# Performance work log

Measured on AMD Instinct MI355X. Metric: run time of the kernel, lower is better.

Reference implementation:

```python
import jax, jax.numpy as jnp
import numpy as np

NPOINT, RADIUS, SIGMA, K = 1024, 0.1, 0.05, 32
KDE_K = 128  # N_points default of kernel_density_estimation_ball


def setup_inputs() -> dict:
    key = jax.random.key(0)
    ks = jax.random.split(key, 9)
    B, N, C = 4, 4096, 16

    def glorot(k, shape):
        fan_in, fan_out = shape
        return jax.random.normal(k, shape, jnp.float32) * jnp.sqrt(2.0 / (fan_in + fan_out))

    return {
        'xyz': jax.random.uniform(ks[0], (B, N, 3), jnp.float32),      # unit cube
        'feature': jax.random.normal(ks[1], (B, N, C), jnp.float32),
        'w_mlp0': glorot(ks[2], (3 + C, 128)),
        'w_mlp1': glorot(ks[3], (128, 128)),
        'w_mlp2': glorot(ks[4], (128, 256)),
        'w_wn': glorot(ks[5], (3, 32)),
        'w_nl0': glorot(ks[6], (1, 16)),
        'w_nl1': glorot(ks[7], (16, 1)),
        'w_np': glorot(ks[8], (32, 256)),
    }


def _pdist2(a, b):
    # squared pairwise distances [B, M, N]
    return (jnp.sum(a * a, -1)[:, :, None] + jnp.sum(b * b, -1)[:, None, :]
            - 2.0 * jnp.einsum('bmd,bnd->bmn', a, b))


def _fps(xyz, npoint):
    # farthest point sampling, seeded at index 0 (matches CUDA op semantics)
    B, N, _ = xyz.shape

    def step(carry, _):
        min_d, last = carry
        p = jnp.take_along_axis(xyz, last[:, None, None], axis=1)  # [B,1,3]
        d = jnp.sum((xyz - p) ** 2, -1)                            # [B,N]
        min_d = jnp.minimum(min_d, d)
        nxt = jnp.argmax(min_d, axis=1).astype(jnp.int32)
        return (min_d, nxt), nxt

    init = (jnp.full((B, N), jnp.inf, xyz.dtype), jnp.zeros((B,), jnp.int32))
    _, rest = jax.lax.scan(step, init, None, length=npoint - 1)
    return jnp.concatenate([jnp.zeros((B, 1), jnp.int32), rest.T], axis=1)  # [B,npoint]


def _ball_query(xyz, radius, k):
    # first-k-in-index-order neighbors with d2 < r^2, padded with first hit
    B, N, _ = xyz.shape
    d2 = _pdist2(xyz, xyz)
    in_ball = d2 < radius * radius                 # self always included
    j = jnp.arange(N, dtype=jnp.int32)
    keys = jnp.where(in_ball, j, j + N)            # in-ball indices sort first
    _, idx = jax.lax.top_k(-keys, k)               # k smallest keys -> positions j
    cnt = jnp.minimum(jnp.sum(in_ball, axis=-1), k)            # [B,N]
    valid = jnp.arange(k) < cnt[..., None]
    idx = jnp.where(valid, idx, idx[..., :1])
    return idx, cnt


def _kde_ball(xyz, radius, sigma, kde_k):
    idx, cnt = _ball_query(xyz, radius, kde_k)     # [B,N,kde_k], [B,N]
    b_ix = jnp.arange(xyz.shape[0])[:, None, None]
    g = xyz[b_ix, idx] - xyz[:, :, None, :]        # [B,N,kde_k,3]
    R = jnp.sqrt(jnp.float32(sigma))
    quad = jnp.sum(jnp.square(g / R), axis=-1)     # [B,N,kde_k]
    mvn = jnp.exp(-0.5 * quad - 3.0 * jnp.log(R) - 1.5 * jnp.log(2.0 * 3.1415926))
    first = mvn[..., :1]
    total = jnp.sum(mvn, axis=-1, keepdims=True)
    cntf = cnt.astype(xyz.dtype)[..., None]
    total = total - first * (jnp.float32(kde_k) - cntf)  # remove padded duplicates
    return total / cntf                             # [B,N,1]


def _knn(k, src, q):
    d2 = _pdist2(q, src)                            # [B,P,N]
    _, idx = jax.lax.top_k(-d2, k)                  # ascending distance
    return idx


def _forward(xyz, feature, w_mlp0, w_mlp1, w_mlp2, w_wn, w_nl0, w_nl1, w_np):
    B = xyz.shape[0]
    conv = lambda x, w: jax.nn.relu(jnp.einsum('bpkc,cf->bpkf', x, w))  # bias-free 1x1 conv

    fps_idx = _fps(xyz, NPOINT)
    new_xyz = jnp.take_along_axis(xyz, fps_idx[..., None], axis=1)      # [B,P,3]

    knn_idx = _knn(K, xyz, new_xyz)                                      # [B,P,K]
    b_ix = jnp.arange(B)[:, None, None]
    grouped_xyz = xyz[b_ix, knn_idx] - new_xyz[:, :, None, :]            # [B,P,K,3]
    grouped_feature = jnp.concatenate([grouped_xyz, feature[b_ix, knn_idx]], axis=-1)

    inv_density = 1.0 / _kde_ball(xyz, RADIUS, SIGMA, KDE_K)             # [B,N,1]
    grouped_density = inv_density[b_ix, knn_idx]                          # [B,P,K,1]
    density_scale = grouped_density / jnp.max(grouped_density, axis=2, keepdims=True)

    h = conv(conv(conv(grouped_feature, w_mlp0), w_mlp1), w_mlp2)        # [B,P,K,256]
    weight = conv(grouped_xyz, w_wn)                                      # [B,P,K,32]
    density_scale = conv(conv(density_scale, w_nl0), w_nl1)               # [B,P,K,1]

    pts = h * density_scale
    pts = jnp.einsum('bpkc,bpkw->bpcw', pts, weight)                      # [B,P,256,32]
    # np_conv: 1x1 kernel with stride [1, mlp[-1]] + VALID -> only c=0 slice survives
    out = jax.nn.relu(jnp.einsum('bpw,wf->bpf', pts[:, :, 0, :], w_np))   # [B,P,256]
    return new_xyz, out


def reference(xyz, feature, w_mlp0, w_mlp1, w_mlp2, w_wn, w_nl0, w_nl1, w_np):
    return _forward(xyz, feature, w_mlp0, w_mlp1, w_mlp2, w_wn, w_nl0, w_nl1, w_np)
```

## Files before the change

kernel.cpp:

```cpp
#include <hip/hip_runtime.h>
#include <math.h>

#pragma clang fp contract(off)

typedef float v2f __attribute__((ext_vector_type(2)));

__global__ __launch_bounds__(256) void prep_kernel(
    const float* __restrict__ xyz, const float* __restrict__ w0,
    const float* __restrict__ w1, const float* __restrict__ w2,
    float* __restrict__ norms, float* __restrict__ W0T,
    float* __restrict__ W1T, float* __restrict__ W2c)
{
    int t = blockIdx.x * 256 + threadIdx.x;
    if (t < 16384) {
        float x = xyz[t*3+0], y = xyz[t*3+1], z = xyz[t*3+2];
        norms[t] = (x*x + y*y) + z*z;
        int c = t >> 7, k = t & 127;
        W1T[c*128 + k] = w1[k*128 + c];
    }
    if (t < 2432) { int c = t / 19, i = t - c*19; W0T[t] = w0[i*128 + c]; }
    if (t < 128)  { W2c[t] = w2[t*256]; }
}

template<int CTRL>
__device__ __forceinline__ double dpp_f64(double v) {
    int lo = __double2loint(v), hi = __double2hiint(v);
    int plo = __builtin_amdgcn_update_dpp(lo, lo, CTRL, 0xF, 0xF, false);
    int phi = __builtin_amdgcn_update_dpp(hi, hi, CTRL, 0xF, 0xF, false);
    return __hiloint2double(phi, plo);
}
template<int CTRL>
__device__ __forceinline__ double max_f64_dpp(double k) {
    return fmax(dpp_f64<CTRL>(k), k);
}
#define KD(md2bits_f, ipi) __hiloint2double(__float_as_int(md2bits_f), (int)(ipi))

__global__ __launch_bounds__(512) void fps_kde_kernel(
    const float* __restrict__ xyz, const float* __restrict__ norms,
    float* __restrict__ new_xyz, float* __restrict__ invden)
{
    __shared__ float4 pts[4096];
    __shared__ float  nxb[3072];
    __shared__ __attribute__((aligned(16))) double swkd[2][4];
    __shared__ float lds_pad[1024];
    int tid = threadIdx.x;
    if (tid == 0x7fffffff) lds_pad[0] = 0.0f;

    if (blockIdx.x < 4) {
        int b = blockIdx.x;
        const float* Xb = xyz + b*12288;
        for (int t = tid; t < 4096; t += 512)
            pts[t] = make_float4(Xb[t*3+0], Xb[t*3+1], Xb[t*3+2], 0.0f);
        __syncthreads();
        if (tid < 256) {
            int lane = tid & 63, wave = tid >> 6;
            v2f Xp[8], Yp[8], Zp[8], md2[8];
            unsigned ip[16];
#pragma unroll
            for (int k = 0; k < 8; ++k) {
                float4 A = pts[(2*k)*256 + tid];
                float4 B = pts[(2*k+1)*256 + tid];
                Xp[k].x = A.x;  Xp[k].y = B.x;
                Yp[k].x = A.y;  Yp[k].y = B.y;
                Zp[k].x = A.z;  Zp[k].y = B.z;
                md2[k].x = INFINITY; md2[k].y = INFINITY;
                ip[2*k]   = ~((unsigned)((2*k)*256 + tid));
                ip[2*k+1] = ~((unsigned)((2*k+1)*256 + tid));
            }
            float cx = pts[0].x, cy = pts[0].y, cz = pts[0].z;
            if (tid == 0) { nxb[0] = cx; nxb[1] = cy; nxb[2] = cz; }
            int buf = 0;
            for (int it = 1; it < 1024; ++it) {
                v2f cx2, cy2, cz2;
                cx2.x = cx; cx2.y = cx;
                cy2.x = cy; cy2.y = cy;
                cz2.x = cz; cz2.y = cz;
#pragma unroll
                for (int k = 0; k < 8; ++k) {
                    v2f dx = Xp[k] - cx2, dy = Yp[k] - cy2, dz = Zp[k] - cz2;
                    v2f dd = (dx*dx + dy*dy) + dz*dz;
                    md2[k] = __builtin_elementwise_min(md2[k], dd);
                }
                double t0 = fmax(fmax(KD(md2[0].x,ip[0]),  KD(md2[0].y,ip[1])),
                                 fmax(KD(md2[1].x,ip[2]),  KD(md2[1].y,ip[3])));
                double t1 = fmax(fmax(KD(md2[2].x,ip[4]),  KD(md2[2].y,ip[5])),
                                 fmax(KD(md2[3].x,ip[6]),  KD(md2[3].y,ip[7])));
                double t2 = fmax(fmax(KD(md2[4].x,ip[8]),  KD(md2[4].y,ip[9])),
                                 fmax(KD(md2[5].x,ip[10]), KD(md2[5].y,ip[11])));
                double t3 = fmax(fmax(KD(md2[6].x,ip[12]), KD(md2[6].y,ip[13])),
                                 fmax(KD(md2[7].x,ip[14]), KD(md2[7].y,ip[15])));
                double key = fmax(fmax(t0, t1), fmax(t2, t3));
                key = max_f64_dpp<0xB1>(key);
                key = max_f64_dpp<0x4E>(key);
                key = max_f64_dpp<0x141>(key);
                key = max_f64_dpp<0x140>(key);
                key = max_f64_dpp<0x142>(key);
                key = max_f64_dpp<0x143>(key);
                if (lane == 63) swkd[buf][wave] = key;
                __syncthreads();
                double2 wab = *((const double2*)&swkd[buf][0]);
                double2 wcd = *((const double2*)&swkd[buf][2]);
                double kk = fmax(fmax(wab.x, wab.y), fmax(wcd.x, wcd.y));
                int fp = (int)(~((unsigned)__double2loint(kk)));
                float4 c = pts[fp];
                cx = c.x; cy = c.y; cz = c.z;
                if (tid == 0) { nxb[it*3+0] = cx; nxb[it*3+1] = cy; nxb[it*3+2] = cz; }
                buf ^= 1;
            }
        } else {
            for (int it = 1; it < 1024; ++it) __syncthreads();
        }
        __syncthreads();
        float* NX = new_xyz + b*3072;
        for (int t = tid; t < 3072; t += 512) NX[t] = nxb[t];
    } else {
        int idx = blockIdx.x - 4;
        int b = idx >> 9;
        int wave = tid >> 6, lane = tid & 63;
        int i_local = ((idx & 511) << 3) + wave;
        const float* Xb = xyz + b*12288;
        const float* Nb = norms + b*4096;
        for (int t = tid; t < 4096; t += 512)
            pts[t] = make_float4(Xb[t*3+0], Xb[t*3+1], Xb[t*3+2], Nb[t]);
        __syncthreads();
        float4 c = pts[i_local];
        const float Rv    = sqrtf(0.05f);
        const float inv_s = 1.0f / (Rv*Rv);
        const float K1    = -3.0f*logf(Rv) - 1.5f*logf(2.0f*3.1415926f);
        float csum = 0.0f; int cnt = 0;
        for (int j = lane; j < 4096; j += 64) {
            float4 q = pts[j];
            float dot = (c.x*q.x + c.y*q.y) + c.z*q.z;
            float t2 = 2.0f * dot;
            float d2 = (c.w + q.w) - t2;
            if (d2 < 0.01f) {
                float gx = q.x - c.x, gy = q.y - c.y, gz = q.z - c.z;
                float dd = (gx*gx + gy*gy) + gz*gz;
                csum += expf(-0.5f * (dd * inv_s) + K1);
                cnt  += 1;
            }
        }
#pragma unroll
        for (int m = 1; m < 64; m <<= 1) {
            csum += __shfl_xor(csum, m, 64);
            cnt  += __shfl_xor(cnt,  m, 64);
        }
        if (lane == 0) {
            float den = csum / (float)cnt;
            invden[b*4096 + i_local] = 1.0f / den;
        }
    }
}

__global__ __launch_bounds__(256) void knn_kernel(
    const float* __restrict__ xyz, const float* __restrict__ norms,
    const float* __restrict__ new_xyz, int* __restrict__ knn_idx)
{
    __shared__ unsigned sd2[4*4096];
    __shared__ int sIdx[4*32];
    int wave = threadIdx.x >> 6, lane = threadIdx.x & 63;
    int qg = blockIdx.x*4 + wave;
    int b = qg >> 10;
    const float* Q = new_xyz + qg*3;
    float qx = Q[0], qy = Q[1], qz = Q[2];
    float nq = (qx*qx + qy*qy) + qz*qz;
    const float* Xb = xyz + b*12288;
    const float* Nb = norms + b*4096;
    unsigned* d2w = sd2 + wave*4096;
    for (int j = lane; j < 4096; j += 64) {
        float x = Xb[j*3+0], y = Xb[j*3+1], z = Xb[j*3+2];
        float dot = (qx*x + qy*y) + qz*z;
        float t2 = 2.0f*dot;
        float d = (nq + Nb[j]) - t2;
        unsigned u = __float_as_uint(d);
        unsigned m = ((unsigned)((int)u >> 31)) | 0x80000000u;
        d2w[j] = u ^ m;
    }
    for (int r = 0; r < 32; ++r) {
        double a0 = -INFINITY, a1 = -INFINITY, a2 = -INFINITY, a3 = -INFINITY;
#pragma unroll
        for (int t = 0; t < 16; ++t) {
            int jb = t*256 + lane*4;
            uint4 v = *((const uint4*)(d2w + jb));
            a0 = fmax(a0, __hiloint2double((int)v.x, jb));
            a1 = fmax(a1, __hiloint2double((int)v.y, jb+1));
            a2 = fmax(a2, __hiloint2double((int)v.z, jb+2));
            a3 = fmax(a3, __hiloint2double((int)v.w, jb+3));
        }
        double key = fmax(fmax(a0, a1), fmax(a2, a3));
        key = max_f64_dpp<0xB1>(key);
        key = max_f64_dpp<0x4E>(key);
        key = max_f64_dpp<0x141>(key);
        key = max_f64_dpp<0x140>(key);
        key = max_f64_dpp<0x142>(key);
        key = max_f64_dpp<0x143>(key);
        int jwin = __builtin_amdgcn_readlane(__double2loint(key), 63);
        if (lane == 0) { sIdx[wave*32 + r] = jwin; d2w[jwin] = 0xFFFFFFFFu; }
    }
    if (lane < 32) knn_idx[qg*32 + lane] = sIdx[wave*32 + lane];
}

__global__ __launch_bounds__(256, 2) void group_mlp_kernel(
    const float* __restrict__ xyz, const float* __restrict__ feat,
    const float* __restrict__ new_xyz, const int* __restrict__ knn_idx,
    const float* __restrict__ invden,
    const float* __restrict__ W0T, const float* __restrict__ W1T,
    const float* __restrict__ W2c, const float* __restrict__ wwn,
    const float* __restrict__ wnl0, const float* __restrict__ wnl1,
    const float* __restrict__ wnp, float* __restrict__ out)
{
    __shared__ float sW1[16384];
    __shared__ float sPW[8][33];
    {
        const float4* g4 = (const float4*)W1T;
        float4* s4 = (float4*)sW1;
#pragma unroll
        for (int i = 0; i < 16; ++i)
            s4[i*256 + threadIdx.x] = g4[i*256 + threadIdx.x];
    }

    int row = blockIdx.x*256 + threadIdx.x;
    int k  = row & 31;
    int pg = row >> 5;
    int b  = row >> 15;
    int j  = knn_idx[row];
    const float* Xb = xyz + b*12288;
    const float* Q  = new_xyz + pg*3;
    float in[19];
    in[0] = Xb[j*3+0] - Q[0];
    in[1] = Xb[j*3+1] - Q[1];
    in[2] = Xb[j*3+2] - Q[2];
    const float4* F = (const float4*)(feat + (size_t)(b*4096 + j)*16);
    float4 f0 = F[0], f1 = F[1], f2 = F[2], f3 = F[3];
    in[3]=f0.x; in[4]=f0.y; in[5]=f0.z; in[6]=f0.w;
    in[7]=f1.x; in[8]=f1.y; in[9]=f1.z; in[10]=f1.w;
    in[11]=f2.x; in[12]=f2.y; in[13]=f2.z; in[14]=f2.w;
    in[15]=f3.x; in[16]=f3.y; in[17]=f3.z; in[18]=f3.w;

    float gd = invden[b*4096 + j];
    float mx = gd;
#pragma unroll
    for (int m = 1; m < 32; m <<= 1) mx = fmaxf(mx, __shfl_xor(mx, m, 64));
    float dsc = gd / mx;
    float sacc = 0.0f;
#pragma unroll
    for (int t = 0; t < 16; ++t)
        sacc = fmaf(fmaxf(dsc * wnl0[t], 0.0f), wnl1[t], sacc);
    float ds = fmaxf(sacc, 0.0f);

    float h1[128];
#pragma unroll
    for (int c = 0; c < 128; ++c) {
        const float* w = W0T + c*19;
        float a = in[0]*w[0];
#pragma unroll
        for (int i = 1; i < 19; ++i) a = fmaf(in[i], w[i], a);
        h1[c] = fmaxf(a, 0.0f);
    }
    __syncthreads();

    float acc0 = 0.0f;
    for (int c2 = 0; c2 < 128; ++c2) {
        const float4* w4 = (const float4*)(sW1 + c2*128);
        float a0 = 0.0f, a1 = 0.0f, a2 = 0.0f, a3 = 0.0f;
#pragma unroll
        for (int kk = 0; kk < 32; ++kk) {
            float4 wv = w4[kk];
            a0 = fmaf(h1[4*kk+0], wv.x, a0);
            a1 = fmaf(h1[4*kk+1], wv.y, a1);
            a2 = fmaf(h1[4*kk+2], wv.z, a2);
            a3 = fmaf(h1[4*kk+3], wv.w, a3);
        }
        float a = (a0+a1) + (a2+a3);
        acc0 = fmaf(fmaxf(a, 0.0f), W2c[c2], acc0);
    }
    float h0 = fmaxf(acc0, 0.0f);
    float s = h0 * ds;

    float gx = in[0], gy = in[1], gz = in[2];
    int l = threadIdx.x >> 5;
#pragma unroll
    for (int w = 0; w < 32; ++w) {
        float a = gx * wwn[w];
        a = fmaf(gy, wwn[32+w], a);
        a = fmaf(gz, wwn[64+w], a);
        float part = s * fmaxf(a, 0.0f);
#pragma unroll
        for (int m = 1; m < 32; m <<= 1) part += __shfl_xor(part, m, 64);
        if (k == 0) sPW[l][w] = part;
    }
    __syncthreads();

    int f = threadIdx.x;
    float wc[32];
#pragma unroll
    for (int w = 0; w < 32; ++w) wc[w] = wnp[w*256 + f];
    int pg0 = blockIdx.x * 8;
#pragma unroll
    for (int r = 0; r < 8; ++r) {
        float a = 0.0f;
#pragma unroll
        for (int w = 0; w < 32; ++w) a = fmaf(sPW[r][w], wc[w], a);
        out[(pg0 + r)*256 + f] = fmaxf(a, 0.0f);
    }
}

extern "C" void kernel_launch(void* const* d_in, const int* in_sizes, int n_in,
                              void* d_out, int out_size, void* d_ws, size_t ws_size,
                              hipStream_t stream) {
    const float* xyz  = (const float*)d_in[0];
    const float* feat = (const float*)d_in[1];
    const float* w0   = (const float*)d_in[2];
    const float* w1   = (const float*)d_in[3];
    const float* w2   = (const float*)d_in[4];
    const float* wwn  = (const float*)d_in[5];
    const float* wnl0 = (const float*)d_in[6];
    const float* wnl1 = (const float*)d_in[7];
    const float* wnp  = (const float*)d_in[8];

    float* out_all  = (float*)d_out;
    float* new_xyz  = out_all;
    float* out2     = out_all + 12288;

    char* ws = (char*)d_ws;
    float* norms  = (float*)(ws + 0);
    float* invden = (float*)(ws + 65536);
    int*   knn    = (int*)  (ws + 131072);
    float* W0T    = (float*)(ws + 655360);
    float* W1T    = (float*)(ws + 665088);
    float* W2c    = (float*)(ws + 730624);

    prep_kernel<<<64, 256, 0, stream>>>(xyz, w0, w1, w2, norms, W0T, W1T, W2c);
    fps_kde_kernel<<<2052, 512, 0, stream>>>(xyz, norms, new_xyz, invden);
    knn_kernel<<<1024, 256, 0, stream>>>(xyz, norms, new_xyz, knn);
    group_mlp_kernel<<<512, 256, 0, stream>>>(xyz, feat, new_xyz, knn, invden,
                                              W0T, W1T, W2c, wwn, wnl0, wnl1,
                                              wnp, out2);
}
```

Before: 795.2 us.

## Keep KNN distance keys in registers and split final projection into separate kernel

The KNN kernel no longer stages 4096 distance keys per query in LDS. Each lane holds 64 packed (distance, index) doubles in registers, loaded with vectorised float4 reads, and each of the 32 selection rounds takes the max among keys strictly below the previous winner. The group MLP kernel now writes per-point 32-wide weighted sums to a workspace buffer, and a new kernel applies the final 32x256 projection, which drops the shared buffer and the block barrier. An unused LDS padding array in fps_kde is also removed. The changes trade LDS traffic and occupancy limits for heavy register pressure (128 VGPRs just for keys) plus an extra launch and a global round trip.

```diff
diff --git a/kernel.cpp b/kernel.cpp
--- a/kernel.cpp
+++ b/kernel.cpp
@@ -42,9 +42,7 @@
     __shared__ float4 pts[4096];
     __shared__ float  nxb[3072];
     __shared__ __attribute__((aligned(16))) double swkd[2][4];
-    __shared__ float lds_pad[1024];
     int tid = threadIdx.x;
-    if (tid == 0x7fffffff) lds_pad[0] = 0.0f;
 
     if (blockIdx.x < 4) {
         int b = blockIdx.x;
@@ -156,8 +154,6 @@
     const float* __restrict__ xyz, const float* __restrict__ norms,
     const float* __restrict__ new_xyz, int* __restrict__ knn_idx)
 {
-    __shared__ unsigned sd2[4*4096];
-    __shared__ int sIdx[4*32];
     int wave = threadIdx.x >> 6, lane = threadIdx.x & 63;
     int qg = blockIdx.x*4 + wave;
     int b = qg >> 10;
@@ -166,38 +162,53 @@
     float nq = (qx*qx + qy*qy) + qz*qz;
     const float* Xb = xyz + b*12288;
     const float* Nb = norms + b*4096;
-    unsigned* d2w = sd2 + wave*4096;
-    for (int j = lane; j < 4096; j += 64) {
-        float x = Xb[j*3+0], y = Xb[j*3+1], z = Xb[j*3+2];
-        float dot = (qx*x + qy*y) + qz*z;
-        float t2 = 2.0f*dot;
-        float d = (nq + Nb[j]) - t2;
-        unsigned u = __float_as_uint(d);
-        unsigned m = ((unsigned)((int)u >> 31)) | 0x80000000u;
-        d2w[j] = u ^ m;
-    }
+
+    double dk[64];
+    int j4 = lane*4;
+#pragma unroll
+    for (int t = 0; t < 16; ++t) {
+        int j0 = t*256 + j4;
+        const float4* X4 = (const float4*)(Xb + j0*3);
+        float4 f0 = X4[0], f1 = X4[1], f2 = X4[2];
+        float4 nn = *((const float4*)(Nb + j0));
+        float xs[4] = {f0.x, f0.w, f1.z, f2.y};
+        float ys[4] = {f0.y, f1.x, f1.w, f2.z};
+        float zs[4] = {f0.z, f1.y, f2.x, f2.w};
+        float ns[4] = {nn.x, nn.y, nn.z, nn.w};
+#pragma unroll
+        for (int e = 0; e < 4; ++e) {
+            float dot = (qx*xs[e] + qy*ys[e]) + qz*zs[e];
+            float t2 = 2.0f*dot;
+            float d = (nq + ns[e]) - t2;
+            unsigned u = __float_as_uint(d);
+            unsigned m = ((unsigned)((int)u >> 31)) | 0x80000000u;
+            dk[t*4 + e] = __hiloint2double((int)(u ^ m), j0 + e);
+        }
+    }
+
+    const double NINF = -INFINITY;
+    double kprev = 0.0;
+    int myj = 0;
+#pragma unroll 1
     for (int r = 0; r < 32; ++r) {
-        double a0 = -INFINITY, a1 = -INFINITY, a2 = -INFINITY, a3 = -INFINITY;
-#pragma unroll
-        for (int t = 0; t < 16; ++t) {
-            int jb = t*256 + lane*4;
-            uint4 v = *((const uint4*)(d2w + jb));
-            a0 = fmax(a0, __hiloint2double((int)v.x, jb));
-            a1 = fmax(a1, __hiloint2double((int)v.y, jb+1));
-            a2 = fmax(a2, __hiloint2double((int)v.z, jb+2));
-            a3 = fmax(a3, __hiloint2double((int)v.w, jb+3));
-        }
-        double key = fmax(fmax(a0, a1), fmax(a2, a3));
-        key = max_f64_dpp<0xB1>(key);
-        key = max_f64_dpp<0x4E>(key);
-        key = max_f64_dpp<0x141>(key);
-        key = max_f64_dpp<0x140>(key);
-        key = max_f64_dpp<0x142>(key);
-        key = max_f64_dpp<0x143>(key);
-        int jwin = __builtin_amdgcn_readlane(__double2loint(key), 63);
-        if (lane == 0) { sIdx[wave*32 + r] = jwin; d2w[jwin] = 0xFFFFFFFFu; }
-    }
-    if (lane < 32) knn_idx[qg*32 + lane] = sIdx[wave*32 + lane];
+        double acc = NINF;
+#pragma unroll
+        for (int i = 0; i < 64; ++i) {
+            double cand = dk[i] < kprev ? dk[i] : NINF;
+            acc = fmax(acc, cand);
+        }
+        acc = max_f64_dpp<0xB1>(acc);
+        acc = max_f64_dpp<0x4E>(acc);
+        acc = max_f64_dpp<0x141>(acc);
+        acc = max_f64_dpp<0x140>(acc);
+        acc = max_f64_dpp<0x142>(acc);
+        acc = max_f64_dpp<0x143>(acc);
+        int wlo = __builtin_amdgcn_readlane(__double2loint(acc), 63);
+        int whi = __builtin_amdgcn_readlane(__double2hiint(acc), 63);
+        kprev = __hiloint2double(whi, wlo);
+        if (lane == r) myj = wlo;
+    }
+    if (lane < 32) knn_idx[qg*32 + lane] = myj;
 }
 
 __global__ __launch_bounds__(256, 2) void group_mlp_kernel(
@@ -207,10 +218,9 @@
     const float* __restrict__ W0T, const float* __restrict__ W1T,
     const float* __restrict__ W2c, const float* __restrict__ wwn,
     const float* __restrict__ wnl0, const float* __restrict__ wnl1,
-    const float* __restrict__ wnp, float* __restrict__ out)
+    float* __restrict__ ptsw)
 {
     __shared__ float sW1[16384];
-    __shared__ float sPW[8][33];
     {
         const float4* g4 = (const float4*)W1T;
         float4* s4 = (float4*)sW1;
@@ -278,7 +288,7 @@
     float s = h0 * ds;
 
     float gx = in[0], gy = in[1], gz = in[2];
-    int l = threadIdx.x >> 5;
+    float* pw = ptsw + pg*32;
 #pragma unroll
     for (int w = 0; w < 32; ++w) {
         float a = gx * wwn[w];
@@ -287,22 +297,21 @@
         float part = s * fmaxf(a, 0.0f);
 #pragma unroll
         for (int m = 1; m < 32; m <<= 1) part += __shfl_xor(part, m, 64);
-        if (k == 0) sPW[l][w] = part;
-    }
-    __syncthreads();
-
-    int f = threadIdx.x;
-    float wc[32];
-#pragma unroll
-    for (int w = 0; w < 32; ++w) wc[w] = wnp[w*256 + f];
-    int pg0 = blockIdx.x * 8;
-#pragma unroll
-    for (int r = 0; r < 8; ++r) {
-        float a = 0.0f;
-#pragma unroll
-        for (int w = 0; w < 32; ++w) a = fmaf(sPW[r][w], wc[w], a);
-        out[(pg0 + r)*256 + f] = fmaxf(a, 0.0f);
-    }
+        if (k == 0) pw[w] = part;
+    }
+}
+
+__global__ __launch_bounds__(256) void final_kernel(
+    const float* __restrict__ ptsw, const float* __restrict__ wnp,
+    float* __restrict__ out)
+{
+    int pg = blockIdx.x;
+    int f  = threadIdx.x;
+    const float* pw = ptsw + pg*32;
+    float a = 0.0f;
+#pragma unroll
+    for (int w = 0; w < 32; ++w) a = fmaf(pw[w], wnp[w*256+f], a);
+    out[pg*256 + f] = fmaxf(a, 0.0f);
 }
 
 extern "C" void kernel_launch(void* const* d_in, const int* in_sizes, int n_in,
@@ -326,14 +335,16 @@
     float* norms  = (float*)(ws + 0);
     float* invden = (float*)(ws + 65536);
     int*   knn    = (int*)  (ws + 131072);
-    float* W0T    = (float*)(ws + 655360);
-    float* W1T    = (float*)(ws + 665088);
-    float* W2c    = (float*)(ws + 730624);
+    float* ptsw   = (float*)(ws + 655360);
+    float* W0T    = (float*)(ws + 1179648);
+    float* W1T    = (float*)(ws + 1189376);
+    float* W2c    = (float*)(ws + 1254912);
 
     prep_kernel<<<64, 256, 0, stream>>>(xyz, w0, w1, w2, norms, W0T, W1T, W2c);
     fps_kde_kernel<<<2052, 512, 0, stream>>>(xyz, norms, new_xyz, invden);
     knn_kernel<<<1024, 256, 0, stream>>>(xyz, norms, new_xyz, knn);
     group_mlp_kernel<<<512, 256, 0, stream>>>(xyz, feat, new_xyz, knn, invden,
                                               W0T, W1T, W2c, wwn, wnl0, wnl1,
-                                              wnp, out2);
-}
+                                              ptsw);
+    final_kernel<<<4096, 256, 0, stream>>>(ptsw, wnp, out2);
+}
```

After: 945.1 us. 1.19x slower.
